# Optimization experiments

Measured on AMD Instinct MI355X. Metric: run time of the kernel, lower is better.

## Reference

```python
import jax, jax.numpy as jnp
import numpy as np

HIDDEN = 128
N_H = 32
E = 262144


def setup_inputs() -> dict:
    key = jax.random.key(0)
    ks = jax.random.split(key, 10)
    s = lambda fan_in: 1.0 / np.sqrt(fan_in)
    return {
        "h_i": jax.random.normal(ks[0], (E, N_H), dtype=jnp.float32),
        "e_ij": jax.random.normal(ks[1], (E, 1), dtype=jnp.float32),
        # lin_A1: 1 -> HIDDEN
        "W_A1": jax.random.uniform(ks[2], (1, HIDDEN), jnp.float32, -s(1), s(1)),
        "b_A1": jnp.zeros((HIDDEN,), jnp.float32),
        # lin_A2: HIDDEN -> N_H*N_H
        "W_A2": jax.random.uniform(ks[3], (HIDDEN, N_H * N_H), jnp.float32, -s(HIDDEN), s(HIDDEN)),
        "b_A2": jnp.zeros((N_H * N_H,), jnp.float32),
        # lin_b1: 1 -> HIDDEN
        "W_b1": jax.random.uniform(ks[4], (1, HIDDEN), jnp.float32, -s(1), s(1)),
        "b_b1": jnp.zeros((HIDDEN,), jnp.float32),
        # lin_b2: HIDDEN -> N_H
        "W_b2": jax.random.uniform(ks[5], (HIDDEN, N_H), jnp.float32, -s(HIDDEN), s(HIDDEN)),
        "b_b2": jnp.zeros((N_H,), jnp.float32),
    }


def reference(h_i, e_ij, W_A1, b_A1, W_A2, b_A2, W_b1, b_b1, W_b2, b_b2):
    # Per-edge MLP producing an [N_H, N_H] matrix A from the scalar edge feature
    A = jax.nn.selu(e_ij @ W_A1 + b_A1)          # [E, HIDDEN]
    A = (A @ W_A2 + b_A2).reshape(-1, N_H, N_H)  # [E, N_H, N_H]
    # Per-edge MLP producing an [N_H] bias b
    b = jax.nn.selu(e_ij @ W_b1 + b_b1)          # [E, HIDDEN]
    b = b @ W_b2 + b_b2                          # [E, N_H]
    # Batched matvec: m_ij[e, i] = sum_j A[e, i, j] * h_i[e, j] + b[e, i]
    m_ij = jnp.einsum('eij,ej->ei', A, h_i) + b
    return m_ij
```

## Files before the change

### kernel.cpp

```cpp
#include <hip/hip_runtime.h>

#define NH        32
#define HID       128
#define E_TOT     262144
#define CH_ELEM   8192
#define NCH_MAIN  16
#define TAIL_OFF  131072
#define TAIL_ELEM 8192

typedef float        f32x4 __attribute__((ext_vector_type(4)));
typedef short        s16x8 __attribute__((ext_vector_type(8)));
typedef unsigned int u32x4 __attribute__((ext_vector_type(4)));

static __device__ __forceinline__ short f2bf(float f) {
    __bf16 b = (__bf16)f;
    return __builtin_bit_cast(short, b);
}
static __device__ __forceinline__ float selu_f(float x) {
    const float kScale  = 1.0507009873554804934193349852946f;
    const float kAlphaS = 1.7580993408473768599402175208123f;
    float neg = kAlphaS * (__expf(x) - 1.0f);
    return x > 0.0f ? kScale * x : neg;
}

__global__ void wt_build(const float* __restrict__ W_A2, const float* __restrict__ b_A2,
                         const float* __restrict__ W_b2, unsigned short* __restrict__ WT) {
    int gid = blockIdx.x * 256 + threadIdx.x;
    if (gid >= TAIL_OFF + TAIL_ELEM) return;
    int it, g, lrow, p, kap;
    if (gid < TAIL_OFF) {
        int c  = gid >> 14;
        int r  = gid & 16383;
        int sl = r >> 10;
        it   = (r >> 9) & 1;
        g    = (r >> 7) & 3;
        lrow = (r >> 3) & 15;
        p    = r & 7;
        kap  = c * 512 + sl * 32 + g * 8 + p;
    } else {
        int r  = gid - TAIL_OFF;
        int sl = r >> 10;
        it   = (r >> 9) & 1;
        g    = (r >> 7) & 3;
        lrow = (r >> 3) & 15;
        p    = r & 7;
        kap  = 4096 + sl * 32 + g * 8 + p;
    }
    int i = it * 16 + lrow;
    float v = 0.0f;
    if (kap < 4096)      v = W_A2[(kap >> 5) * 1024 + i * 32 + (kap & 31)];
    else if (kap < 4128) v = b_A2[i * 32 + (kap - 4096)];
    else if (kap < 4256) v = W_b2[(kap - 4128) * 32 + i];
    WT[gid] = (unsigned short)f2bf(v);
}

__global__ void __launch_bounds__(256, 4)
msg_main(const float* __restrict__ h_i, const float* __restrict__ e_ij,
         const float* __restrict__ W_A1, const float* __restrict__ b_A1,
         const float* __restrict__ W_b1, const float* __restrict__ b_b1,
         const float* __restrict__ b_b2,
         const unsigned short* __restrict__ WT,
         float* __restrict__ out)
{
    __shared__ float cA1[HID], cBA1[HID], cB1a[HID], cB1b[HID], cb2[NH];

    const int tid  = threadIdx.x;
    const int lane = tid & 63;
    const int wid  = tid >> 6;
    const int lrow = lane & 15;
    const int g    = lane >> 4;
    const int e0   = blockIdx.x * 256 + wid * 64;

    if (tid < HID) {
        cA1[tid]  = W_A1[tid];
        cBA1[tid] = b_A1[tid];
        cB1a[tid] = W_b1[tid];
        cB1b[tid] = b_b1[tid];
    }
    if (tid < NH) cb2[tid] = b_b2[tid];

    const float ev_own = e_ij[e0 + lane];

    s16x8 hb[4];
    #pragma unroll
    for (int ct = 0; ct < 4; ++ct) {
        int er = e0 + ct * 16 + lrow;
        const float* hp = h_i + er * 32 + g * 8;
        f32x4 h0 = *(const f32x4*)hp;
        f32x4 h1 = *(const f32x4*)(hp + 4);
        #pragma unroll
        for (int p = 0; p < 4; ++p) {
            hb[ct][p]     = f2bf(h0[p]);
            hb[ct][p + 4] = f2bf(h1[p]);
        }
    }

    float ev_ct[4];
    #pragma unroll
    for (int ct = 0; ct < 4; ++ct) ev_ct[ct] = __shfl(ev_own, ct * 16 + lrow);

    f32x4 acc[4][2];
    #pragma unroll
    for (int ct = 0; ct < 4; ++ct)
        #pragma unroll
        for (int it = 0; it < 2; ++it)
            acc[ct][it] = (f32x4){0.f, 0.f, 0.f, 0.f};
    const f32x4 zf = (f32x4){0.f, 0.f, 0.f, 0.f};

    float u_own[8];

    __syncthreads();

    const unsigned short* wbase = WT + lane * 8;

    for (int c = 0; c < NCH_MAIN; ++c) {
        #pragma unroll
        for (int sl = 0; sl < 8; ++sl) {
            int s = c * 8 + sl;
            u_own[sl] = selu_f(fmaf(ev_own, cA1[s], cBA1[s]));
        }

        #pragma unroll
        for (int sl = 0; sl < 8; ++sl) {
            const unsigned short* wp = wbase + c * CH_ELEM + sl * 1024;
            u32x4 r0 = *(const u32x4*)(wp);
            u32x4 r1 = *(const u32x4*)(wp + 512);
            s16x8 A0 = __builtin_bit_cast(s16x8, r0);
            s16x8 A1 = __builtin_bit_cast(s16x8, r1);
            f32x4 u4[4];
            #pragma unroll
            for (int ct = 0; ct < 4; ++ct) {
                float uv = __shfl(u_own[sl], ct * 16 + lrow);
                u4[ct] = (f32x4){uv, uv, uv, uv};
            }
            {
                f32x4 t[4];
                #pragma unroll
                for (int ct = 0; ct < 4; ++ct)
                    t[ct] = __builtin_amdgcn_mfma_f32_16x16x32_bf16(A0, hb[ct], zf, 0, 0, 0);
                #pragma unroll
                for (int ct = 0; ct < 4; ++ct)
                    acc[ct][0] = __builtin_elementwise_fma(t[ct], u4[ct], acc[ct][0]);
            }
            {
                f32x4 t[4];
                #pragma unroll
                for (int ct = 0; ct < 4; ++ct)
                    t[ct] = __builtin_amdgcn_mfma_f32_16x16x32_bf16(A1, hb[ct], zf, 0, 0, 0);
                #pragma unroll
                for (int ct = 0; ct < 4; ++ct)
                    acc[ct][1] = __builtin_elementwise_fma(t[ct], u4[ct], acc[ct][1]);
            }
        }
    }

    {
        const unsigned short* wp = wbase + TAIL_OFF;
        u32x4 r0 = *(const u32x4*)(wp);
        u32x4 r1 = *(const u32x4*)(wp + 512);
        s16x8 A0 = __builtin_bit_cast(s16x8, r0);
        s16x8 A1 = __builtin_bit_cast(s16x8, r1);
        #pragma unroll
        for (int ct = 0; ct < 4; ++ct) {
            acc[ct][0] = __builtin_amdgcn_mfma_f32_16x16x32_bf16(A0, hb[ct], acc[ct][0], 0, 0, 0);
            acc[ct][1] = __builtin_amdgcn_mfma_f32_16x16x32_bf16(A1, hb[ct], acc[ct][1], 0, 0, 0);
        }
    }
    #pragma unroll
    for (int q = 0; q < 4; ++q) {
        const unsigned short* wp = wbase + TAIL_OFF + (q + 1) * 1024;
        u32x4 r0 = *(const u32x4*)(wp);
        u32x4 r1 = *(const u32x4*)(wp + 512);
        s16x8 A0 = __builtin_bit_cast(s16x8, r0);
        s16x8 A1 = __builtin_bit_cast(s16x8, r1);
        int tb = q * 32 + g * 8;
        f32x4 wb0 = *(const f32x4*)&cB1a[tb];
        f32x4 wb1 = *(const f32x4*)&cB1a[tb + 4];
        f32x4 bb0 = *(const f32x4*)&cB1b[tb];
        f32x4 bb1 = *(const f32x4*)&cB1b[tb + 4];
        #pragma unroll
        for (int ct = 0; ct < 4; ++ct) {
            s16x8 B;
            #pragma unroll
            for (int p = 0; p < 4; ++p) {
                B[p]     = f2bf(selu_f(fmaf(ev_ct[ct], wb0[p], bb0[p])));
                B[p + 4] = f2bf(selu_f(fmaf(ev_ct[ct], wb1[p], bb1[p])));
            }
            acc[ct][0] = __builtin_amdgcn_mfma_f32_16x16x32_bf16(A0, B, acc[ct][0], 0, 0, 0);
            acc[ct][1] = __builtin_amdgcn_mfma_f32_16x16x32_bf16(A1, B, acc[ct][1], 0, 0, 0);
        }
    }

    #pragma unroll
    for (int it = 0; it < 2; ++it) {
        f32x4 b2v = *(const f32x4*)&cb2[it * 16 + g * 4];
        #pragma unroll
        for (int ct = 0; ct < 4; ++ct) {
            int edge = e0 + ct * 16 + lrow;
            f32x4 vo = acc[ct][it] + b2v;
            *(f32x4*)&out[edge * 32 + it * 16 + g * 4] = vo;
        }
    }
}

extern "C" void kernel_launch(void* const* d_in, const int* in_sizes, int n_in,
                              void* d_out, int out_size, void* d_ws, size_t ws_size,
                              hipStream_t stream) {
    const float* h_i  = (const float*)d_in[0];
    const float* e_ij = (const float*)d_in[1];
    const float* W_A1 = (const float*)d_in[2];
    const float* b_A1 = (const float*)d_in[3];
    const float* W_A2 = (const float*)d_in[4];
    const float* b_A2 = (const float*)d_in[5];
    const float* W_b1 = (const float*)d_in[6];
    const float* b_b1 = (const float*)d_in[7];
    const float* W_b2 = (const float*)d_in[8];
    const float* b_b2 = (const float*)d_in[9];

    unsigned short* WT = (unsigned short*)d_ws;

    wt_build<<<(TAIL_OFF + TAIL_ELEM + 255) / 256, 256, 0, stream>>>(W_A2, b_A2, W_b2, WT);
    msg_main<<<E_TOT / 256, 256, 0, stream>>>(h_i, e_ij, W_A1, b_A1, W_b1, b_b1,
                                              b_b2, WT, (float*)d_out);
}
```

Measured before the change: 98.04 us.

## Switch per-edge matvec to 32x32x16 bf16 MFMA with reorganized weight layout

Replaces the 16x16x32 MFMA tiling (4 edge tiles by 2 output halves) with 32x32x16 MFMA over 2 edge tiles of 32, and rebuilds the bf16 weight table layout to match the new operand ordering. The intent is to issue fewer, larger MFMAs and fewer selu-scaling FMA passes per hidden unit. It also lowers the occupancy hint from 4 to 3 waves per SIMD to allow more registers for the 16-wide accumulators. The output store pattern changes to 4-row groups per lane.

```diff
diff --git a/kernel.cpp b/kernel.cpp
--- a/kernel.cpp
+++ b/kernel.cpp
@@ -8,9 +8,10 @@
 #define TAIL_OFF  131072
 #define TAIL_ELEM 8192
 
-typedef float        f32x4 __attribute__((ext_vector_type(4)));
-typedef short        s16x8 __attribute__((ext_vector_type(8)));
-typedef unsigned int u32x4 __attribute__((ext_vector_type(4)));
+typedef float        f32x4  __attribute__((ext_vector_type(4)));
+typedef float        f32x16 __attribute__((ext_vector_type(16)));
+typedef short        s16x8  __attribute__((ext_vector_type(8)));
+typedef unsigned int u32x4  __attribute__((ext_vector_type(4)));
 
 static __device__ __forceinline__ short f2bf(float f) {
     __bf16 b = (__bf16)f;
@@ -27,34 +28,36 @@
                          const float* __restrict__ W_b2, unsigned short* __restrict__ WT) {
     int gid = blockIdx.x * 256 + threadIdx.x;
     if (gid >= TAIL_OFF + TAIL_ELEM) return;
-    int it, g, lrow, p, kap;
+    float v = 0.0f;
     if (gid < TAIL_OFF) {
-        int c  = gid >> 14;
-        int r  = gid & 16383;
+        int c  = gid >> 13;
+        int r  = gid & 8191;
         int sl = r >> 10;
-        it   = (r >> 9) & 1;
-        g    = (r >> 7) & 3;
-        lrow = (r >> 3) & 15;
-        p    = r & 7;
-        kap  = c * 512 + sl * 32 + g * 8 + p;
+        int jh = (r >> 9) & 1;
+        int l  = (r >> 3) & 63;
+        int p  = r & 7;
+        int i  = l & 31;
+        int kap = c * 256 + sl * 32 + jh * 16 + ((l >> 5) << 3) + p;
+        v = W_A2[(kap >> 5) * 1024 + i * 32 + (kap & 31)];
     } else {
         int r  = gid - TAIL_OFF;
         int sl = r >> 10;
-        it   = (r >> 9) & 1;
-        g    = (r >> 7) & 3;
-        lrow = (r >> 3) & 15;
-        p    = r & 7;
-        kap  = 4096 + sl * 32 + g * 8 + p;
-    }
-    int i = it * 16 + lrow;
-    float v = 0.0f;
-    if (kap < 4096)      v = W_A2[(kap >> 5) * 1024 + i * 32 + (kap & 31)];
-    else if (kap < 4128) v = b_A2[i * 32 + (kap - 4096)];
-    else if (kap < 4256) v = W_b2[(kap - 4128) * 32 + i];
+        int jh = (r >> 9) & 1;
+        int l  = (r >> 3) & 63;
+        int p  = r & 7;
+        int i  = l & 31;
+        if (sl == 0) {
+            int j = jh * 16 + ((l >> 5) << 3) + p;
+            v = b_A2[i * 32 + j];
+        } else if (sl <= 4) {
+            int t = (sl - 1) * 32 + jh * 16 + ((l >> 5) << 3) + p;
+            v = W_b2[t * 32 + i];
+        }
+    }
     WT[gid] = (unsigned short)f2bf(v);
 }
 
-__global__ void __launch_bounds__(256, 4)
+__global__ void __launch_bounds__(256, 3)
 msg_main(const float* __restrict__ h_i, const float* __restrict__ e_ij,
          const float* __restrict__ W_A1, const float* __restrict__ b_A1,
          const float* __restrict__ W_b1, const float* __restrict__ b_b1,
@@ -67,8 +70,8 @@
     const int tid  = threadIdx.x;
     const int lane = tid & 63;
     const int wid  = tid >> 6;
-    const int lrow = lane & 15;
-    const int g    = lane >> 4;
+    const int el   = lane & 31;
+    const int kh   = lane >> 5;
     const int e0   = blockIdx.x * 256 + wid * 64;
 
     if (tid < HID) {
@@ -81,31 +84,33 @@
 
     const float ev_own = e_ij[e0 + lane];
 
-    s16x8 hb[4];
-    #pragma unroll
-    for (int ct = 0; ct < 4; ++ct) {
-        int er = e0 + ct * 16 + lrow;
-        const float* hp = h_i + er * 32 + g * 8;
-        f32x4 h0 = *(const f32x4*)hp;
-        f32x4 h1 = *(const f32x4*)(hp + 4);
-        #pragma unroll
-        for (int p = 0; p < 4; ++p) {
-            hb[ct][p]     = f2bf(h0[p]);
-            hb[ct][p + 4] = f2bf(h1[p]);
-        }
-    }
-
-    float ev_ct[4];
-    #pragma unroll
-    for (int ct = 0; ct < 4; ++ct) ev_ct[ct] = __shfl(ev_own, ct * 16 + lrow);
-
-    f32x4 acc[4][2];
-    #pragma unroll
-    for (int ct = 0; ct < 4; ++ct)
-        #pragma unroll
-        for (int it = 0; it < 2; ++it)
-            acc[ct][it] = (f32x4){0.f, 0.f, 0.f, 0.f};
-    const f32x4 zf = (f32x4){0.f, 0.f, 0.f, 0.f};
+    s16x8 hb[2][2];
+    #pragma unroll
+    for (int et = 0; et < 2; ++et) {
+        int er = e0 + et * 32 + el;
+        #pragma unroll
+        for (int jh = 0; jh < 2; ++jh) {
+            const float* hp = h_i + er * 32 + jh * 16 + kh * 8;
+            f32x4 h0 = *(const f32x4*)hp;
+            f32x4 h1 = *(const f32x4*)(hp + 4);
+            #pragma unroll
+            for (int p = 0; p < 4; ++p) {
+                hb[et][jh][p]     = f2bf(h0[p]);
+                hb[et][jh][p + 4] = f2bf(h1[p]);
+            }
+        }
+    }
+
+    float ev2[2];
+    #pragma unroll
+    for (int et = 0; et < 2; ++et) ev2[et] = __shfl(ev_own, et * 32 + el);
+
+    f32x16 acc0, acc1;
+    #pragma unroll
+    for (int k = 0; k < 16; ++k) { acc0[k] = 0.f; acc1[k] = 0.f; }
+    f32x16 zf16;
+    #pragma unroll
+    for (int k = 0; k < 16; ++k) zf16[k] = 0.f;
 
     float u_own[8];
 
@@ -123,82 +128,75 @@
         #pragma unroll
         for (int sl = 0; sl < 8; ++sl) {
             const unsigned short* wp = wbase + c * CH_ELEM + sl * 1024;
-            u32x4 r0 = *(const u32x4*)(wp);
-            u32x4 r1 = *(const u32x4*)(wp + 512);
-            s16x8 A0 = __builtin_bit_cast(s16x8, r0);
-            s16x8 A1 = __builtin_bit_cast(s16x8, r1);
-            f32x4 u4[4];
-            #pragma unroll
-            for (int ct = 0; ct < 4; ++ct) {
-                float uv = __shfl(u_own[sl], ct * 16 + lrow);
-                u4[ct] = (f32x4){uv, uv, uv, uv};
-            }
-            {
-                f32x4 t[4];
-                #pragma unroll
-                for (int ct = 0; ct < 4; ++ct)
-                    t[ct] = __builtin_amdgcn_mfma_f32_16x16x32_bf16(A0, hb[ct], zf, 0, 0, 0);
-                #pragma unroll
-                for (int ct = 0; ct < 4; ++ct)
-                    acc[ct][0] = __builtin_elementwise_fma(t[ct], u4[ct], acc[ct][0]);
-            }
-            {
-                f32x4 t[4];
-                #pragma unroll
-                for (int ct = 0; ct < 4; ++ct)
-                    t[ct] = __builtin_amdgcn_mfma_f32_16x16x32_bf16(A1, hb[ct], zf, 0, 0, 0);
-                #pragma unroll
-                for (int ct = 0; ct < 4; ++ct)
-                    acc[ct][1] = __builtin_elementwise_fma(t[ct], u4[ct], acc[ct][1]);
-            }
+            u32x4 a0 = *(const u32x4*)(wp);
+            u32x4 a1 = *(const u32x4*)(wp + 512);
+            s16x8 A0 = __builtin_bit_cast(s16x8, a0);
+            s16x8 A1 = __builtin_bit_cast(s16x8, a1);
+            float uv0 = __shfl(u_own[sl], el);
+            float uv1 = __shfl(u_own[sl], 32 + el);
+            f32x16 t0 = __builtin_amdgcn_mfma_f32_32x32x16_bf16(A0, hb[0][0], zf16, 0, 0, 0);
+            f32x16 t1 = __builtin_amdgcn_mfma_f32_32x32x16_bf16(A0, hb[1][0], zf16, 0, 0, 0);
+            t0 = __builtin_amdgcn_mfma_f32_32x32x16_bf16(A1, hb[0][1], t0, 0, 0, 0);
+            t1 = __builtin_amdgcn_mfma_f32_32x32x16_bf16(A1, hb[1][1], t1, 0, 0, 0);
+            f32x16 u0, u1;
+            #pragma unroll
+            for (int k = 0; k < 16; ++k) { u0[k] = uv0; u1[k] = uv1; }
+            acc0 = __builtin_elementwise_fma(t0, u0, acc0);
+            acc1 = __builtin_elementwise_fma(t1, u1, acc1);
         }
     }
 
     {
         const unsigned short* wp = wbase + TAIL_OFF;
-        u32x4 r0 = *(const u32x4*)(wp);
-        u32x4 r1 = *(const u32x4*)(wp + 512);
-        s16x8 A0 = __builtin_bit_cast(s16x8, r0);
-        s16x8 A1 = __builtin_bit_cast(s16x8, r1);
-        #pragma unroll
-        for (int ct = 0; ct < 4; ++ct) {
-            acc[ct][0] = __builtin_amdgcn_mfma_f32_16x16x32_bf16(A0, hb[ct], acc[ct][0], 0, 0, 0);
-            acc[ct][1] = __builtin_amdgcn_mfma_f32_16x16x32_bf16(A1, hb[ct], acc[ct][1], 0, 0, 0);
-        }
+        u32x4 a0 = *(const u32x4*)(wp);
+        u32x4 a1 = *(const u32x4*)(wp + 512);
+        s16x8 A0 = __builtin_bit_cast(s16x8, a0);
+        s16x8 A1 = __builtin_bit_cast(s16x8, a1);
+        acc0 = __builtin_amdgcn_mfma_f32_32x32x16_bf16(A0, hb[0][0], acc0, 0, 0, 0);
+        acc1 = __builtin_amdgcn_mfma_f32_32x32x16_bf16(A0, hb[1][0], acc1, 0, 0, 0);
+        acc0 = __builtin_amdgcn_mfma_f32_32x32x16_bf16(A1, hb[0][1], acc0, 0, 0, 0);
+        acc1 = __builtin_amdgcn_mfma_f32_32x32x16_bf16(A1, hb[1][1], acc1, 0, 0, 0);
     }
     #pragma unroll
     for (int q = 0; q < 4; ++q) {
         const unsigned short* wp = wbase + TAIL_OFF + (q + 1) * 1024;
-        u32x4 r0 = *(const u32x4*)(wp);
-        u32x4 r1 = *(const u32x4*)(wp + 512);
-        s16x8 A0 = __builtin_bit_cast(s16x8, r0);
-        s16x8 A1 = __builtin_bit_cast(s16x8, r1);
-        int tb = q * 32 + g * 8;
-        f32x4 wb0 = *(const f32x4*)&cB1a[tb];
-        f32x4 wb1 = *(const f32x4*)&cB1a[tb + 4];
-        f32x4 bb0 = *(const f32x4*)&cB1b[tb];
-        f32x4 bb1 = *(const f32x4*)&cB1b[tb + 4];
-        #pragma unroll
-        for (int ct = 0; ct < 4; ++ct) {
-            s16x8 B;
+        u32x4 a0 = *(const u32x4*)(wp);
+        u32x4 a1 = *(const u32x4*)(wp + 512);
+        s16x8 A0 = __builtin_bit_cast(s16x8, a0);
+        s16x8 A1 = __builtin_bit_cast(s16x8, a1);
+        #pragma unroll
+        for (int jh = 0; jh < 2; ++jh) {
+            int tb = q * 32 + jh * 16 + kh * 8;
+            f32x4 wb0 = *(const f32x4*)&cB1a[tb];
+            f32x4 wb1 = *(const f32x4*)&cB1a[tb + 4];
+            f32x4 bb0 = *(const f32x4*)&cB1b[tb];
+            f32x4 bb1 = *(const f32x4*)&cB1b[tb + 4];
+            s16x8 B0, B1;
             #pragma unroll
             for (int p = 0; p < 4; ++p) {
-                B[p]     = f2bf(selu_f(fmaf(ev_ct[ct], wb0[p], bb0[p])));
-                B[p + 4] = f2bf(selu_f(fmaf(ev_ct[ct], wb1[p], bb1[p])));
+                B0[p]     = f2bf(selu_f(fmaf(ev2[0], wb0[p], bb0[p])));
+                B0[p + 4] = f2bf(selu_f(fmaf(ev2[0], wb1[p], bb1[p])));
+                B1[p]     = f2bf(selu_f(fmaf(ev2[1], wb0[p], bb0[p])));
+                B1[p + 4] = f2bf(selu_f(fmaf(ev2[1], wb1[p], bb1[p])));
             }
-            acc[ct][0] = __builtin_amdgcn_mfma_f32_16x16x32_bf16(A0, B, acc[ct][0], 0, 0, 0);
-            acc[ct][1] = __builtin_amdgcn_mfma_f32_16x16x32_bf16(A1, B, acc[ct][1], 0, 0, 0);
-        }
-    }
-
-    #pragma unroll
-    for (int it = 0; it < 2; ++it) {
-        f32x4 b2v = *(const f32x4*)&cb2[it * 16 + g * 4];
-        #pragma unroll
-        for (int ct = 0; ct < 4; ++ct) {
-            int edge = e0 + ct * 16 + lrow;
-            f32x4 vo = acc[ct][it] + b2v;
-            *(f32x4*)&out[edge * 32 + it * 16 + g * 4] = vo;
+            s16x8 A = jh == 0 ? A0 : A1;
+            acc0 = __builtin_amdgcn_mfma_f32_32x32x16_bf16(A, B0, acc0, 0, 0, 0);
+            acc1 = __builtin_amdgcn_mfma_f32_32x32x16_bf16(A, B1, acc1, 0, 0, 0);
+        }
+    }
+
+    #pragma unroll
+    for (int et = 0; et < 2; ++et) {
+        int edge = e0 + et * 32 + el;
+        const f32x16& a = et == 0 ? acc0 : acc1;
+        #pragma unroll
+        for (int rq = 0; rq < 4; ++rq) {
+            int row0 = rq * 8 + kh * 4;
+            f32x4 b2v = *(const f32x4*)&cb2[row0];
+            f32x4 vo;
+            #pragma unroll
+            for (int m = 0; m < 4; ++m) vo[m] = a[rq * 4 + m] + b2v[m];
+            *(f32x4*)&out[edge * 32 + row0] = vo;
         }
     }
 }
```

Measured after the change: 98.35 us. No clear change (+0.3%).
